# Kernel optimization log

Hardware: AMD Instinct MI355X
Metric: run time of the kernel (lower is better)

Reference implementation:

```python
import jax, jax.numpy as jnp
import numpy as np

N_HEADS = 16
N_EMBED = 1024
HEAD_SIZE = 64


def setup_inputs() -> dict:
    key = jax.random.key(0)
    ks = jax.random.split(key, 6)
    B, T, C = 2, 2048, N_EMBED
    x = jax.random.normal(ks[0], (B, T, C), dtype=jnp.float32)
    s = 1.0 / np.sqrt(C)
    Wq = jax.random.normal(ks[1], (N_HEADS, C, HEAD_SIZE), dtype=jnp.float32) * s
    Wk = jax.random.normal(ks[2], (N_HEADS, C, HEAD_SIZE), dtype=jnp.float32) * s
    Wv = jax.random.normal(ks[3], (N_HEADS, C, HEAD_SIZE), dtype=jnp.float32) * s
    Wo = jax.random.normal(ks[4], (C, C), dtype=jnp.float32) * s
    bo = jax.random.normal(ks[5], (C,), dtype=jnp.float32) * 0.01
    return {"x": x, "Wq": Wq, "Wk": Wk, "Wv": Wv, "Wo": Wo, "bo": bo}


def reference(x, Wq, Wk, Wv, Wo, bo):
    B, T, C = x.shape
    # per-head projections: [B, H, T, D]
    q = jnp.einsum('btc,hcd->bhtd', x, Wq)
    k = jnp.einsum('btc,hcd->bhtd', x, Wk)
    v = jnp.einsum('btc,hcd->bhtd', x, Wv)
    # NOTE: original scales by n_embed**0.5 (C), not head_size**0.5
    scores = jnp.einsum('bhtd,bhsd->bhts', q, k) / jnp.sqrt(jnp.float32(C))
    causal = jnp.tril(jnp.ones((T, T), dtype=bool))
    scores = jnp.where(causal, scores, -jnp.inf)
    wei = jax.nn.softmax(scores, axis=-1)
    out = jnp.einsum('bhts,bhsd->bhtd', wei, v)  # [B, H, T, D]
    out = out.transpose(0, 2, 1, 3).reshape(B, T, C)  # concat heads
    return out @ Wo.T + bo
```

## Files before the change

kernel.cpp:

```cpp
#include <hip/hip_runtime.h>


#define Bsz 2
#define Tsz 2048
#define Cdim 1024
#define Hn 16
#define Dh 64

typedef short bf16x8 __attribute__((ext_vector_type(8)));
typedef float f32x4 __attribute__((ext_vector_type(4)));
typedef unsigned short u16;

#define MFMA(a, b, c) __builtin_amdgcn_mfma_f32_16x16x32_bf16(a, b, c, 0, 0, 0)
#define NEGINF (-__builtin_inff())
#define EXP2(x) __builtin_amdgcn_exp2f(x)

#define GLD16(g, l)                                                            \
  __builtin_amdgcn_global_load_lds((const __attribute__((address_space(1))) void*)(g), \
                                   (__attribute__((address_space(3))) void*)(l), 16, 0, 0)

__device__ __forceinline__ u16 f2bf(float f) {
  unsigned u = __builtin_bit_cast(unsigned, f);
  unsigned r = 0x7fffu + ((u >> 16) & 1u);
  return (u16)((u + r) >> 16);
}

__device__ __forceinline__ unsigned cvtpk(float lo, float hi) {
  unsigned r;
  asm("v_cvt_pk_bf16_f32 %0, %1, %2" : "=v"(r) : "v"(lo), "v"(hi));
  return r;
}

__global__ __launch_bounds__(256) void k_cast_x(const float* __restrict__ x,
                                                u16* __restrict__ xb, int n4) {
  int i = blockIdx.x * 256 + threadIdx.x;
  if (i >= n4) return;
  float4 v = reinterpret_cast<const float4*>(x)[i];
  ushort4 o;
  o.x = f2bf(v.x); o.y = f2bf(v.y); o.z = f2bf(v.z); o.w = f2bf(v.w);
  reinterpret_cast<ushort4*>(xb)[i] = o;
}

__global__ __launch_bounds__(256) void k_cast_w(const float* __restrict__ Wq,
                                                const float* __restrict__ Wk,
                                                const float* __restrict__ Wv,
                                                u16* __restrict__ wt) {
  __shared__ u16 tile[64][68];
  const int mh = blockIdx.y;
  const int m = mh >> 4, h = mh & 15;
  const float* src = (m == 0 ? Wq : m == 1 ? Wk : Wv) + (size_t)h * Cdim * Dh;
  const int c0 = blockIdx.x * 64;
  const int tid = threadIdx.x;
  const int cc = tid >> 4, d4 = (tid & 15) * 4;
#pragma unroll
  for (int i = 0; i < 4; ++i) {
    int c = i * 16 + cc;
    float4 v = *(const float4*)(src + (size_t)(c0 + c) * Dh + d4);
    tile[d4 + 0][c] = f2bf(v.x);
    tile[d4 + 1][c] = f2bf(v.y);
    tile[d4 + 2][c] = f2bf(v.z);
    tile[d4 + 3][c] = f2bf(v.w);
  }
  __syncthreads();
  const int c4 = (tid & 15) * 4, dd = tid >> 4;
#pragma unroll
  for (int i = 0; i < 4; ++i) {
    int d = i * 16 + dd;
    ushort4 o;
    o.x = tile[d][c4]; o.y = tile[d][c4 + 1];
    o.z = tile[d][c4 + 2]; o.w = tile[d][c4 + 3];
    *(ushort4*)(wt + (size_t)(mh * 64 + d) * Cdim + c0 + c4) = o;
  }
}

__global__ __launch_bounds__(256) void k_gemm_qkv(const u16* __restrict__ xb,
                                                  const u16* __restrict__ wt,
                                                  u16* __restrict__ qb,
                                                  u16* __restrict__ kb,
                                                  u16* __restrict__ vtb) {
  __shared__ __align__(16) u16 As[3][4096], Bs[3][4096];
  const int tid = threadIdx.x, lane = tid & 63, wid = tid >> 6;
  const int cl = lane & 15, kg = lane >> 4;
  const int row0 = blockIdx.y * 128, col0 = blockIdx.x * 128;
  const int wrow = (wid >> 1) * 64, wcol = (wid & 1) * 64;
  f32x4 acc[4][4] = {};
  const int csrc = ((lane & 3) ^ ((lane >> 3) & 3)) * 8;
  const u16* a_src = xb + (size_t)(row0 + 32 * wid + (lane >> 2)) * Cdim + csrc;
  const u16* b_src = wt + (size_t)(col0 + 32 * wid + (lane >> 2)) * Cdim + csrc;

  auto stage = [&](int buf, int ke) {
    u16* Ad = &As[buf][1024 * wid];
    u16* Bd = &Bs[buf][1024 * wid];
    GLD16(a_src + ke, Ad);
    GLD16(a_src + 16 * Cdim + ke, Ad + 512);
    GLD16(b_src + ke, Bd);
    GLD16(b_src + 16 * Cdim + ke, Bd + 512);
  };

  const int rdswz = (kg ^ ((cl >> 1) & 3)) * 8;

  stage(0, 0);
  stage(1, 32);
  stage(2, 64);
  for (int kk = 0; kk < 32; ++kk) {
    if (kk < 30)
      asm volatile("s_waitcnt vmcnt(8)" ::: "memory");
    else if (kk == 30)
      asm volatile("s_waitcnt vmcnt(4)" ::: "memory");
    else
      asm volatile("s_waitcnt vmcnt(0)" ::: "memory");
    __builtin_amdgcn_s_barrier();
    const int cur = kk % 3;
    const u16* ar = &As[cur][(wrow + cl) * 32 + rdswz];
    const u16* br = &Bs[cur][(wcol + cl) * 32 + rdswz];
    bf16x8 af[4], bfr[4];
#pragma unroll
    for (int mi = 0; mi < 4; ++mi) af[mi] = *(const bf16x8*)(ar + mi * 512);
#pragma unroll
    for (int ni = 0; ni < 4; ++ni) bfr[ni] = *(const bf16x8*)(br + ni * 512);
#pragma unroll
    for (int mi = 0; mi < 4; ++mi)
#pragma unroll
      for (int ni = 0; ni < 4; ++ni)
        acc[mi][ni] = MFMA(af[mi], bfr[ni], acc[mi][ni]);
    __builtin_amdgcn_s_barrier();
    if (kk + 3 < 32) stage(cur, (kk + 3) * 32);
  }
#pragma unroll
  for (int mi = 0; mi < 4; ++mi) {
#pragma unroll
    for (int ni = 0; ni < 4; ++ni) {
      int n = col0 + wcol + ni * 16 + cl;
      int m = n >> 10, h = (n >> 6) & 15, d = n & 63;
#pragma unroll
      for (int j = 0; j < 4; ++j) {
        int r = row0 + wrow + mi * 16 + kg * 4 + j;
        int b = r >> 11, t = r & 2047;
        float av = acc[mi][ni][j];
        if (m == 0) av *= 0.04508422f;
        u16 v = f2bf(av);
        size_t bh = (size_t)(b * Hn + h);
        if (m == 0)
          qb[(bh * Tsz + t) * Dh + d] = v;
        else if (m == 1)
          kb[(bh * Tsz + t) * Dh + d] = v;
        else
          vtb[(bh * Dh + d) * Tsz + t] = v;
      }
    }
  }
}

__global__ __launch_bounds__(256, 4) void k_attn(const u16* __restrict__ qb,
                                                 const u16* __restrict__ kb,
                                                 const u16* __restrict__ vtb,
                                                 u16* __restrict__ ob) {
  __shared__ __align__(16) u16 KV[2][8192];
  __shared__ __align__(16) u16 Plds[4][1024];
  const int lane = threadIdx.x & 63, wid = threadIdx.x >> 6;
  const int cl = lane & 15, kg = lane >> 4;
  const int s = blockIdx.x >> 3;
  const int t = 31 - (s >> 2);
  const int p = (blockIdx.x & 7) + 8 * (s & 3);
  const int h = p & 15, b = p >> 4;
  const int qr = t * 64 + wid * 16;
  const size_t bh = (size_t)(b * Hn + h);
  const u16* Qp = qb + bh * Tsz * Dh;
  const u16* Kp = kb + bh * Tsz * Dh;
  const u16* Vp = vtb + bh * Dh * Tsz;

  const u16* pk_src[2];
  const u16* pv_src[2];
#pragma unroll
  for (int c = 0; c < 2; ++c) {
    int lo = c * 4096 + wid * 1024 + lane * 16;
    int r = lo >> 7, cb = lo & 127;
    int cbs = cb ^ ((r & 7) << 4);
    pk_src[c] = Kp + r * Dh + (cbs >> 1);
    pv_src[c] = Vp + (size_t)r * Tsz + (cbs >> 1);
  }

  auto stage = [&](int buf, int kt) {
    GLD16(pk_src[0] + kt * 4096, &KV[buf][(wid * 1024) >> 1]);
    GLD16(pk_src[1] + kt * 4096, &KV[buf][(4096 + wid * 1024) >> 1]);
    GLD16(pv_src[0] + kt * 64, &KV[buf][(8192 + wid * 1024) >> 1]);
    GLD16(pv_src[1] + kt * 64, &KV[buf][(12288 + wid * 1024) >> 1]);
  };

  bf16x8 qa0 = *(const bf16x8*)(Qp + (size_t)(qr + cl) * Dh + kg * 8);
  bf16x8 qa1 = *(const bf16x8*)(Qp + (size_t)(qr + cl) * Dh + 32 + kg * 8);

  f32x4 o[4] = {};
  float m = NEGINF, l = 0.f;

  char* pb = (char*)&Plds[wid][0];
  const int rdoff0 = ((cl << 7) + (kg << 4)) ^ ((cl & 7) << 4);
  const int rdoff1 = ((cl << 7) + 64 + (kg << 4)) ^ ((cl & 7) << 4);
  const int rowoff = wid * 16;
  const int swz0 = (kg * 16) ^ ((cl & 7) << 4);
  const int swz1 = (kg * 16 + 64) ^ ((cl & 7) << 4);

  stage(0, 0);
  __syncthreads();
  int cur = 0;
  for (int kt = 0; kt <= t; ++kt) {
    if (kt < t) stage(cur ^ 1, kt + 1);
    char* kvb = (char*)&KV[cur][0];
    bf16x8 ka[8];
#pragma unroll
    for (int nt = 0; nt < 4; ++nt) {
      int rbase = (nt * 16 + cl) << 7;
      ka[nt * 2] = *(const bf16x8*)(kvb + rbase + swz0);
      ka[nt * 2 + 1] = *(const bf16x8*)(kvb + rbase + swz1);
    }
    f32x4 sv[4];
    __builtin_amdgcn_s_setprio(1);
#pragma unroll
    for (int nt = 0; nt < 4; ++nt) {
      f32x4 z = {};
      z = MFMA(ka[nt * 2], qa0, z);
      z = MFMA(ka[nt * 2 + 1], qa1, z);
      sv[nt] = z;
    }
    __builtin_amdgcn_s_setprio(0);
    bf16x8 vf[8];
#pragma unroll
    for (int dt = 0; dt < 4; ++dt) {
      int rbase = 8192 + ((dt * 16 + cl) << 7);
      vf[dt * 2] = *(const bf16x8*)(kvb + rbase + swz0);
      vf[dt * 2 + 1] = *(const bf16x8*)(kvb + rbase + swz1);
    }
    if (kt == t) {
#pragma unroll
      for (int nt = 0; nt < 4; ++nt)
#pragma unroll
        for (int j = 0; j < 4; ++j)
          if (nt * 16 + kg * 4 + j > rowoff + cl) sv[nt][j] = NEGINF;
    }
    float tm = fmaxf(fmaxf(fmaxf(sv[0][0], sv[0][1]), fmaxf(sv[0][2], sv[0][3])),
                     fmaxf(fmaxf(sv[1][0], sv[1][1]), fmaxf(sv[1][2], sv[1][3])));
    tm = fmaxf(tm, fmaxf(fmaxf(fmaxf(sv[2][0], sv[2][1]), fmaxf(sv[2][2], sv[2][3])),
                         fmaxf(fmaxf(sv[3][0], sv[3][1]), fmaxf(sv[3][2], sv[3][3]))));
    if (!__all(tm <= m + 8.0f)) {
      tm = fmaxf(tm, __shfl_xor(tm, 16));
      tm = fmaxf(tm, __shfl_xor(tm, 32));
      float mnew = fmaxf(m, tm);
      float corr = EXP2(m - mnew);
      m = mnew;
      l *= corr;
      float c0 = __shfl(corr, kg * 4 + 0);
      float c1 = __shfl(corr, kg * 4 + 1);
      float c2 = __shfl(corr, kg * 4 + 2);
      float c3 = __shfl(corr, kg * 4 + 3);
#pragma unroll
      for (int dt = 0; dt < 4; ++dt) {
        o[dt][0] *= c0; o[dt][1] *= c1; o[dt][2] *= c2; o[dt][3] *= c3;
      }
    }
    float rs = 0.f;
#pragma unroll
    for (int nt = 0; nt < 4; ++nt)
#pragma unroll
      for (int j = 0; j < 4; ++j) {
        float pv = EXP2(sv[nt][j] - m);
        sv[nt][j] = pv;
        rs += pv;
      }
    l += rs;
#pragma unroll
    for (int nt = 0; nt < 4; ++nt) {
      uint2 pk;
      pk.x = cvtpk(sv[nt][0], sv[nt][1]);
      pk.y = cvtpk(sv[nt][2], sv[nt][3]);
      int waddr = ((cl << 7) + (nt << 5) + (kg << 3)) ^ ((cl & 7) << 4);
      *(uint2*)(pb + waddr) = pk;
    }
    bf16x8 pa0 = *(const bf16x8*)(pb + rdoff0);
    bf16x8 pa1 = *(const bf16x8*)(pb + rdoff1);
    __builtin_amdgcn_s_setprio(1);
#pragma unroll
    for (int dt = 0; dt < 4; ++dt) {
      o[dt] = MFMA(pa0, vf[dt * 2], o[dt]);
      o[dt] = MFMA(pa1, vf[dt * 2 + 1], o[dt]);
    }
    __builtin_amdgcn_s_setprio(0);
    __syncthreads();
    cur ^= 1;
  }

  l += __shfl_xor(l, 16);
  l += __shfl_xor(l, 32);
  float i0 = 1.f / __shfl(l, kg * 4 + 0), i1 = 1.f / __shfl(l, kg * 4 + 1);
  float i2 = 1.f / __shfl(l, kg * 4 + 2), i3 = 1.f / __shfl(l, kg * 4 + 3);
  float inv[4] = {i0, i1, i2, i3};
#pragma unroll
  for (int dt = 0; dt < 4; ++dt)
#pragma unroll
    for (int j = 0; j < 4; ++j) {
      int tr = qr + kg * 4 + j;
      ob[(size_t)(b * Tsz + tr) * Cdim + h * Dh + dt * 16 + cl] = f2bf(o[dt][j] * inv[j]);
    }
}

__global__ __launch_bounds__(256) void k_gemm_out(const u16* __restrict__ ob,
                                                  const u16* __restrict__ wob,
                                                  const float* __restrict__ bo,
                                                  float* __restrict__ out) {
  __shared__ __align__(16) u16 As[3][4096], Bs[3][2048];
  const int tid = threadIdx.x, lane = tid & 63, wid = tid >> 6;
  const int cl = lane & 15, kg = lane >> 4;
  const int row0 = blockIdx.y * 128, col0 = blockIdx.x * 64;
  const int wrow = (wid >> 1) * 64, wcol = (wid & 1) * 32;
  f32x4 acc[4][2] = {};
  const int csrc = ((lane & 3) ^ ((lane >> 3) & 3)) * 8;
  const u16* a_src = ob + (size_t)(row0 + 32 * wid + (lane >> 2)) * Cdim + csrc;
  const u16* b_src = wob + (size_t)(col0 + 16 * wid + (lane >> 2)) * Cdim + csrc;

  auto stage = [&](int buf, int ke) {
    u16* Ad = &As[buf][1024 * wid];
    u16* Bd = &Bs[buf][512 * wid];
    GLD16(a_src + ke, Ad);
    GLD16(a_src + 16 * Cdim + ke, Ad + 512);
    GLD16(b_src + ke, Bd);
  };

  const int rdswz = (kg ^ ((cl >> 1) & 3)) * 8;

  stage(0, 0);
  stage(1, 32);
  stage(2, 64);
  for (int kk = 0; kk < 32; ++kk) {
    if (kk < 30)
      asm volatile("s_waitcnt vmcnt(6)" ::: "memory");
    else if (kk == 30)
      asm volatile("s_waitcnt vmcnt(3)" ::: "memory");
    else
      asm volatile("s_waitcnt vmcnt(0)" ::: "memory");
    __builtin_amdgcn_s_barrier();
    const int cur = kk % 3;
    const u16* ar = &As[cur][(wrow + cl) * 32 + rdswz];
    const u16* br = &Bs[cur][(wcol + cl) * 32 + rdswz];
    bf16x8 af[4], bfr[2];
#pragma unroll
    for (int mi = 0; mi < 4; ++mi) af[mi] = *(const bf16x8*)(ar + mi * 512);
#pragma unroll
    for (int ni = 0; ni < 2; ++ni) bfr[ni] = *(const bf16x8*)(br + ni * 512);
#pragma unroll
    for (int mi = 0; mi < 4; ++mi)
#pragma unroll
      for (int ni = 0; ni < 2; ++ni)
        acc[mi][ni] = MFMA(af[mi], bfr[ni], acc[mi][ni]);
    __builtin_amdgcn_s_barrier();
    if (kk + 3 < 32) stage(cur, (kk + 3) * 32);
  }
#pragma unroll
  for (int mi = 0; mi < 4; ++mi) {
#pragma unroll
    for (int ni = 0; ni < 2; ++ni) {
      int n = col0 + wcol + ni * 16 + cl;
      float bias = bo[n];
#pragma unroll
      for (int j = 0; j < 4; ++j) {
        int r = row0 + wrow + mi * 16 + kg * 4 + j;
        out[(size_t)r * Cdim + n] = acc[mi][ni][j] + bias;
      }
    }
  }
}

extern "C" void kernel_launch(void* const* d_in, const int* in_sizes, int n_in,
                              void* d_out, int out_size, void* d_ws, size_t ws_size,
                              hipStream_t stream) {
  (void)in_sizes; (void)n_in; (void)out_size; (void)ws_size;
  const float* x = (const float*)d_in[0];
  const float* Wq = (const float*)d_in[1];
  const float* Wk = (const float*)d_in[2];
  const float* Wv = (const float*)d_in[3];
  const float* Wo = (const float*)d_in[4];
  const float* bo = (const float*)d_in[5];
  float* out = (float*)d_out;
  char* ws = (char*)d_ws;
  u16* xb = (u16*)(ws);
  u16* wt = (u16*)(ws + (8u << 20));
  u16* wob = (u16*)(ws + (14u << 20));
  u16* qb = (u16*)(ws + (16u << 20));
  u16* kb = (u16*)(ws + (24u << 20));
  u16* vtb = (u16*)(ws + (32u << 20));
  u16* ob = (u16*)(ws + (40u << 20));

  k_cast_x<<<4096, 256, 0, stream>>>(x, xb, Bsz * Tsz * Cdim / 4);
  k_cast_x<<<1024, 256, 0, stream>>>(Wo, wob, Cdim * Cdim / 4);
  k_cast_w<<<dim3(16, 48), 256, 0, stream>>>(Wq, Wk, Wv, wt);
  k_gemm_qkv<<<dim3(24, 32), 256, 0, stream>>>(xb, wt, qb, kb, vtb);
  k_attn<<<1024, 256, 0, stream>>>(qb, kb, vtb, ob);
  k_gemm_out<<<dim3(16, 32), 256, 0, stream>>>(ob, wob, bo, out);
}
```

Before: 112.5 us.

## Remap GEMM block indices for XCD-local tile grouping and merge cast launches

After: 113.8 us. No clear change (+1.2%).

```diff
diff --git a/kernel.cpp b/kernel.cpp
--- a/kernel.cpp
+++ b/kernel.cpp
@@ -31,14 +31,24 @@
   return r;
 }
 
-__global__ __launch_bounds__(256) void k_cast_x(const float* __restrict__ x,
-                                                u16* __restrict__ xb, int n4) {
+__global__ __launch_bounds__(256) void k_cast_xw(const float* __restrict__ x,
+                                                 u16* __restrict__ xb, int n4x,
+                                                 const float* __restrict__ wo,
+                                                 u16* __restrict__ wob, int n4w) {
   int i = blockIdx.x * 256 + threadIdx.x;
-  if (i >= n4) return;
-  float4 v = reinterpret_cast<const float4*>(x)[i];
+  const float* s;
+  u16* d;
+  if (i < n4x) {
+    s = x; d = xb;
+  } else {
+    i -= n4x;
+    if (i >= n4w) return;
+    s = wo; d = wob;
+  }
+  float4 v = reinterpret_cast<const float4*>(s)[i];
   ushort4 o;
   o.x = f2bf(v.x); o.y = f2bf(v.y); o.z = f2bf(v.z); o.w = f2bf(v.w);
-  reinterpret_cast<ushort4*>(xb)[i] = o;
+  reinterpret_cast<ushort4*>(d)[i] = o;
 }
 
 __global__ __launch_bounds__(256) void k_cast_w(const float* __restrict__ Wq,
@@ -81,7 +91,10 @@
   __shared__ __align__(16) u16 As[3][4096], Bs[3][4096];
   const int tid = threadIdx.x, lane = tid & 63, wid = tid >> 6;
   const int cl = lane & 15, kg = lane >> 4;
-  const int row0 = blockIdx.y * 128, col0 = blockIdx.x * 128;
+  const int j = blockIdx.x & 7, mb = blockIdx.x >> 3;
+  const int bx = (j & 1) * 12 + (mb % 12);
+  const int by = (j >> 1) * 8 + (mb / 12);
+  const int row0 = by * 128, col0 = bx * 128;
   const int wrow = (wid >> 1) * 64, wcol = (wid & 1) * 64;
   f32x4 acc[4][4] = {};
   const int csrc = ((lane & 3) ^ ((lane >> 3) & 3)) * 8;
@@ -133,10 +146,10 @@
       int n = col0 + wcol + ni * 16 + cl;
       int m = n >> 10, h = (n >> 6) & 15, d = n & 63;
 #pragma unroll
-      for (int j = 0; j < 4; ++j) {
-        int r = row0 + wrow + mi * 16 + kg * 4 + j;
+      for (int j2 = 0; j2 < 4; ++j2) {
+        int r = row0 + wrow + mi * 16 + kg * 4 + j2;
         int b = r >> 11, t = r & 2047;
-        float av = acc[mi][ni][j];
+        float av = acc[mi][ni][j2];
         if (m == 0) av *= 0.04508422f;
         u16 v = f2bf(av);
         size_t bh = (size_t)(b * Hn + h);
@@ -309,7 +322,10 @@
   __shared__ __align__(16) u16 As[3][4096], Bs[3][2048];
   const int tid = threadIdx.x, lane = tid & 63, wid = tid >> 6;
   const int cl = lane & 15, kg = lane >> 4;
-  const int row0 = blockIdx.y * 128, col0 = blockIdx.x * 64;
+  const int j = blockIdx.x & 7, mb = blockIdx.x >> 3;
+  const int bx = (j & 1) * 8 + (mb % 8);
+  const int by = (j >> 1) * 8 + (mb / 8);
+  const int row0 = by * 128, col0 = bx * 64;
   const int wrow = (wid >> 1) * 64, wcol = (wid & 1) * 32;
   f32x4 acc[4][2] = {};
   const int csrc = ((lane & 3) ^ ((lane >> 3) & 3)) * 8;
@@ -360,9 +376,9 @@
       int n = col0 + wcol + ni * 16 + cl;
       float bias = bo[n];
 #pragma unroll
-      for (int j = 0; j < 4; ++j) {
-        int r = row0 + wrow + mi * 16 + kg * 4 + j;
-        out[(size_t)r * Cdim + n] = acc[mi][ni][j] + bias;
+      for (int j2 = 0; j2 < 4; ++j2) {
+        int r = row0 + wrow + mi * 16 + kg * 4 + j2;
+        out[(size_t)r * Cdim + n] = acc[mi][ni][j2] + bias;
       }
     }
   }
@@ -388,10 +404,10 @@
   u16* vtb = (u16*)(ws + (32u << 20));
   u16* ob = (u16*)(ws + (40u << 20));
 
-  k_cast_x<<<4096, 256, 0, stream>>>(x, xb, Bsz * Tsz * Cdim / 4);
-  k_cast_x<<<1024, 256, 0, stream>>>(Wo, wob, Cdim * Cdim / 4);
+  const int n4x = Bsz * Tsz * Cdim / 4, n4w = Cdim * Cdim / 4;
+  k_cast_xw<<<(n4x + n4w + 255) / 256, 256, 0, stream>>>(x, xb, n4x, Wo, wob, n4w);
   k_cast_w<<<dim3(16, 48), 256, 0, stream>>>(Wq, Wk, Wv, wt);
-  k_gemm_qkv<<<dim3(24, 32), 256, 0, stream>>>(xb, wt, qb, kb, vtb);
+  k_gemm_qkv<<<768, 256, 0, stream>>>(xb, wt, qb, kb, vtb);
   k_attn<<<1024, 256, 0, stream>>>(qb, kb, vtb, ob);
-  k_gemm_out<<<dim3(16, 32), 256, 0, stream>>>(ob, wob, bo, out);
-}
+  k_gemm_out<<<512, 256, 0, stream>>>(ob, wob, bo, out);
+}
```
